# Optimization experiments

Hardware: AMD Instinct MI355X
Metric: run time of the kernel (lower is better)

Reference implementation:

```python
import jax, jax.numpy as jnp
import numpy as np


def log_g(x):
    # log of g(x) = where(x>=0, x+0.5, sigmoid(x)), computed stably in log space
    return jnp.where(x >= 0, jnp.log(jax.nn.relu(x) + 0.5), -jax.nn.softplus(-x))


def setup_inputs() -> dict:
    key = jax.random.key(0)
    k1, k2 = jax.random.split(key)
    B, S, D = 4, 4096, 1024
    x = jax.random.normal(k1, (B, S, D), dtype=jnp.float32)
    W_hg = jax.random.normal(k2, (2 * D, D), dtype=jnp.float32) * (1.0 / np.sqrt(D))
    return {"x": x, "W_hg": W_hg}


def reference(x, W_hg):
    # x: [B, S, D], W_hg: [2D, D]
    hg = jnp.einsum('bsd,ed->bse', x, W_hg)  # [B, S, 2D]
    hidden, gate = jnp.split(hg, 2, axis=-1)

    log_coeffs = -jax.nn.softplus(gate)       # log(1 - z)
    log_z = -jax.nn.softplus(-gate)            # log(z)
    log_values = log_z + log_g(hidden)

    # Heinsen associative scan in log space along seq axis
    a_star = jnp.cumsum(log_coeffs, axis=1)
    log_h0_plus_b_star = jax.lax.cumlogsumexp(log_values - a_star, axis=1)
    log_h = a_star + log_h0_plus_b_star
    out = jnp.exp(log_h)  # [B, S, D]; to_out is Identity (expansion_factor=1.0)
    return out
```

## Files before the change

### kernel.cpp

```cpp
#include <hip/hip_runtime.h>
#include <stdint.h>

#define B_ 4
#define S_ 4096
#define D_ 1024
#define E_ 2048
#define K_ 1024
#define M_ (B_*S_)
#define SEG 64
#define NSEG (S_/SEG)

typedef __bf16 bf16x8 __attribute__((ext_vector_type(8)));
typedef float  f32x4  __attribute__((ext_vector_type(4)));
typedef _Float16 f16x2 __attribute__((ext_vector_type(2)));

__device__ __forceinline__ unsigned short f2bf(float f) {
    union { float f; unsigned int u; } x; x.f = f;
    unsigned int u = x.u;
    return (unsigned short)((u + 0x7fffu + ((u >> 16) & 1u)) >> 16);
}

__device__ __forceinline__ void gload16(const void* g, void* l) {
    __builtin_amdgcn_global_load_lds(
        (const __attribute__((address_space(1))) void*)(uintptr_t)g,
        (__attribute__((address_space(3))) void*)(uintptr_t)l,
        16, 0, 0);
}

__device__ __forceinline__ unsigned int packCV(float hid, float gat) {
    float e  = __expf(gat);
    float c  = __builtin_amdgcn_rcpf(1.f + e);
    float gg = (hid >= 0.f) ? (hid + 0.5f)
                            : __builtin_amdgcn_rcpf(1.f + __expf(-hid));
    float v  = (1.f - c) * gg;
    union { f16x2 h; unsigned int u; } pk;
    pk.h[0] = (_Float16)c; pk.h[1] = (_Float16)v;
    return pk.u;
}

__global__ void cvt_xw(const float* __restrict__ x, unsigned short* __restrict__ xb,
                       const float* __restrict__ w, unsigned short* __restrict__ wb) {
    int b = blockIdx.x;
    if (b < 16384) {
        int i = (b * 256 + threadIdx.x) * 4;
        float4 f = *(const float4*)(x + i);
        ushort4 o;
        o.x = f2bf(f.x); o.y = f2bf(f.y); o.z = f2bf(f.z); o.w = f2bf(f.w);
        *(ushort4*)(xb + i) = o;
    } else {
        int i = ((b - 16384) * 256 + threadIdx.x) * 4;
        int r = i >> 10;
        int k = i & 1023;
        int d = r >> 1, g = r & 1;
        const float* src = w + (size_t)(g * D_ + d) * K_ + k;
        float4 f = *(const float4*)src;
        ushort4 o;
        o.x = f2bf(f.x); o.y = f2bf(f.y); o.z = f2bf(f.z); o.w = f2bf(f.w);
        *(ushort4*)(wb + i) = o;
    }
}

#define BM 128
#define BN 128
#define BK 32

__global__ __launch_bounds__(256, 2)
void gemm_ep(const unsigned short* __restrict__ xb,
             const unsigned short* __restrict__ wb,
             unsigned int* __restrict__ cv,
             float2* __restrict__ segCV) {
    __shared__ unsigned short As[BM * BK];
    __shared__ unsigned short Bs[BN * BK];
    __shared__ __align__(16) unsigned int Ep[4][64][36];

    const int l    = blockIdx.x;
    const int xcd  = l & 7;
    const int r    = l >> 3;
    const int sub  = r >> 6;
    const int win  = r & 63;
    const int eB   = (sub & 1) * 8 + (win & 7);
    const int mB   = xcd * 16 + (sub >> 1) * 8 + (win >> 3);
    const int mBase = mB * BM;
    const int eBase = eB * BN;

    const int tid  = threadIdx.x;
    const int lane = tid & 63;
    const int w    = tid >> 6;
    const int waveM = (w >> 1) * 64;
    const int waveN = (w & 1) * 64;

    f32x4 acc[4][4] = {};

    const int row0 = tid >> 2, cu = tid & 3;
    const unsigned short* aG0 = xb + (size_t)(mBase + row0) * K_ + cu * 8;
    const unsigned short* aG1 = aG0 + (size_t)64 * K_;
    const unsigned short* bG0 = wb + (size_t)(eBase + row0) * K_ + cu * 8;
    const unsigned short* bG1 = bG0 + (size_t)64 * K_;
    unsigned short* aL0 = As + (size_t)(w * 64) * 8;
    unsigned short* aL1 = As + (size_t)(256 + w * 64) * 8;
    unsigned short* bL0 = Bs + (size_t)(w * 64) * 8;
    unsigned short* bL1 = Bs + (size_t)(256 + w * 64) * 8;

    const int mrow = lane & 15;
    const int kg   = (lane >> 4) * 8;

    for (int k0 = 0; k0 < K_; k0 += BK) {
        __syncthreads();
        gload16(aG0 + k0, aL0);
        gload16(aG1 + k0, aL1);
        gload16(bG0 + k0, bL0);
        gload16(bG1 + k0, bL1);
        __syncthreads();

        bf16x8 af[4], bfr[4];
#pragma unroll
        for (int i = 0; i < 4; i++)
            af[i] = *(const bf16x8*)(As + (size_t)(waveM + i * 16 + mrow) * BK + kg);
#pragma unroll
        for (int j = 0; j < 4; j++)
            bfr[j] = *(const bf16x8*)(Bs + (size_t)(waveN + j * 16 + mrow) * BK + kg);
#pragma unroll
        for (int i = 0; i < 4; i++)
#pragma unroll
            for (int j = 0; j < 4; j++)
                acc[i][j] = __builtin_amdgcn_mfma_f32_16x16x32_bf16(af[i], bfr[j], acc[i][j], 0, 0, 0);
    }

    const int q    = lane >> 4;
    const int odd  = lane & 1;
    const int colL = (lane & 15) >> 1;
    unsigned int* EpW = &Ep[w][0][0];

#pragma unroll
    for (int i = 0; i < 4; i++) {
#pragma unroll
        for (int j = 0; j < 4; j++) {
            float o0 = __shfl_xor(acc[i][j][0], 1, 64);
            float o1 = __shfl_xor(acc[i][j][1], 1, 64);
            float o2 = __shfl_xor(acc[i][j][2], 1, 64);
            float o3 = __shfl_xor(acc[i][j][3], 1, 64);
            float m0 = odd ? acc[i][j][2] : acc[i][j][0];
            float m1 = odd ? acc[i][j][3] : acc[i][j][1];
            float p0 = odd ? o2 : o0;
            float p1 = odd ? o3 : o1;
            float h0 = odd ? p0 : m0, g0 = odd ? m0 : p0;
            float h1 = odd ? p1 : m1, g1 = odd ? m1 : p1;
            int row = i * 16 + q * 4 + odd * 2;
            int col = j * 8 + colL;
            EpW[(row    ) * 36 + col] = packCV(h0, g0);
            EpW[(row + 1) * 36 + col] = packCV(h1, g1);
        }
    }
    const int srow = lane >> 3;
    const int schk = lane & 7;
    const size_t dBaseS = (size_t)((eBase + waveN) >> 1) + schk * 4;
#pragma unroll
    for (int gph = 0; gph < 8; gph++) {
        int row = gph * 8 + srow;
        uint4 valq = *(const uint4*)&EpW[row * 36 + schk * 4];
        size_t m = (size_t)(mBase + waveM + row);
        *(uint4*)(cv + m * D_ + dBaseS) = valq;
    }

    __syncthreads();
    float* scratch = (float*)As;

    {
        const int dl = tid & 63;
        const int qt = tid >> 6;
        const int wq = (qt >> 1) * 2 + (dl >> 5);
        const int rBase = (qt & 1) * 32;
        const int c = dl & 31;
        const unsigned int* src = &Ep[wq][rBase][c];
        float C = 1.f, V = 0.f;
#pragma unroll 8
        for (int rr = 0; rr < 32; rr++) {
            union { unsigned int u; f16x2 h; } uu;
            uu.u = src[rr * 36];
            float cc = (float)uu.h[0], vv = (float)uu.h[1];
            V = fmaf(cc, V, vv);
            C *= cc;
        }
        scratch[(qt * 64 + dl) * 2 + 0] = C;
        scratch[(qt * 64 + dl) * 2 + 1] = V;
    }
    __syncthreads();
    if (tid < 128) {
        const int k  = tid >> 6;
        const int dl = tid & 63;
        float C0 = scratch[((2 * k    ) * 64 + dl) * 2 + 0];
        float V0 = scratch[((2 * k    ) * 64 + dl) * 2 + 1];
        float C1 = scratch[((2 * k + 1) * 64 + dl) * 2 + 0];
        float V1 = scratch[((2 * k + 1) * 64 + dl) * 2 + 1];
        int bj = mB * 2 + k;
        int dg = (eBase >> 1) + dl;
        segCV[(size_t)bj * D_ + dg] = make_float2(C0 * C1, fmaf(C1, V0, V1));
    }
}

__global__ void seg_scan(const float2* __restrict__ segCV, float* __restrict__ segH) {
    int b = blockIdx.x;
    int d = blockIdx.y * 256 + threadIdx.x;
    float h = 0.f;
    for (int j0 = 0; j0 < NSEG; j0 += 8) {
        float2 s[8];
#pragma unroll
        for (int t = 0; t < 8; t++)
            s[t] = segCV[(size_t)(b * NSEG + j0 + t) * D_ + d];
#pragma unroll
        for (int t = 0; t < 8; t++) {
            segH[(size_t)(b * NSEG + j0 + t) * D_ + d] = h;
            h = fmaf(s[t].x, h, s[t].y);
        }
    }
}

__global__ void seg_apply(const uint2* __restrict__ cv2,
                          const float2* __restrict__ segH2, float2* __restrict__ out2) {
    const int bj = blockIdx.x;
    const int p  = blockIdx.y * 256 + threadIdx.x;

    float2 hs = segH2[(size_t)bj * (D_ / 2) + p];
    float h0 = hs.x, h1 = hs.y;
    size_t base = (size_t)bj * SEG * (D_ / 2) + p;
    for (int s0 = 0; s0 < SEG; s0 += 8) {
        uint2 u[8];
#pragma unroll
        for (int t = 0; t < 8; t++)
            u[t] = cv2[base + (size_t)(s0 + t) * (D_ / 2)];
        float2 o[8];
#pragma unroll
        for (int t = 0; t < 8; t++) {
            union { unsigned int u; f16x2 h; } a, b; a.u = u[t].x; b.u = u[t].y;
            h0 = fmaf((float)a.h[0], h0, (float)a.h[1]);
            h1 = fmaf((float)b.h[0], h1, (float)b.h[1]);
            o[t] = make_float2(h0, h1);
        }
#pragma unroll
        for (int t = 0; t < 8; t++)
            out2[base + (size_t)(s0 + t) * (D_ / 2)] = o[t];
    }
}

extern "C" void kernel_launch(void* const* d_in, const int* in_sizes, int n_in,
                              void* d_out, int out_size, void* d_ws, size_t ws_size,
                              hipStream_t stream) {
    const float* x = (const float*)d_in[0];
    const float* wmat = (const float*)d_in[1];
    float* out = (float*)d_out;
    char* ws = (char*)d_ws;

    unsigned short* xb = (unsigned short*)(ws);
    unsigned short* wb = (unsigned short*)(ws + (32u << 20));
    unsigned int*   cv = (unsigned int*)(ws + (36u << 20));
    float2*      segCV = (float2*)(ws + (100u << 20));
    float*        segH = (float*)(ws + (102u << 20));

    cvt_xw<<<18432, 256, 0, stream>>>(x, xb, wmat, wb);

    gemm_ep<<<2048, 256, 0, stream>>>(xb, wb, cv, segCV);

    dim3 gs(B_, D_ / 256);
    seg_scan<<<gs, 256, 0, stream>>>((const float2*)segCV, segH);

    dim3 ga(B_ * NSEG, D_ / 512);
    seg_apply<<<ga, 256, 0, stream>>>((const uint2*)cv, (const float2*)segH,
                                      (float2*)out);
}
```

Baseline: 232.5 us.

## Fuse scan into GEMM epilogue using cross-block decoupled lookback chain

The separate segment-scan and apply kernels are removed. Each GEMM block now publishes its 128-row aggregate (C,V) to a global array with release atomics, waits on all earlier row-blocks of the same batch and channel group, and writes the final output straight from LDS. This drops the cv intermediate write/read round trip and two kernel launches. In exchange it adds serial spin-waiting between blocks that depends on dispatch order, with a risk of stalls or deadlock if earlier blocks are not resident, and the block order no longer follows the previous XCD-aware L2 swizzle.

```diff
diff --git a/kernel.cpp b/kernel.cpp
--- a/kernel.cpp
+++ b/kernel.cpp
@@ -7,8 +7,8 @@
 #define E_ 2048
 #define K_ 1024
 #define M_ (B_*S_)
-#define SEG 64
-#define NSEG (S_/SEG)
+#define NCHAIN 32
+#define SENT 0xFFFFFFFFFFFFFFFFull
 
 typedef __bf16 bf16x8 __attribute__((ext_vector_type(8)));
 typedef float  f32x4  __attribute__((ext_vector_type(4)));
@@ -39,7 +39,8 @@
 }
 
 __global__ void cvt_xw(const float* __restrict__ x, unsigned short* __restrict__ xb,
-                       const float* __restrict__ w, unsigned short* __restrict__ wb) {
+                       const float* __restrict__ w, unsigned short* __restrict__ wb,
+                       unsigned long long* __restrict__ segAgg) {
     int b = blockIdx.x;
     if (b < 16384) {
         int i = (b * 256 + threadIdx.x) * 4;
@@ -47,7 +48,7 @@
         ushort4 o;
         o.x = f2bf(f.x); o.y = f2bf(f.y); o.z = f2bf(f.z); o.w = f2bf(f.w);
         *(ushort4*)(xb + i) = o;
-    } else {
+    } else if (b < 18432) {
         int i = ((b - 16384) * 256 + threadIdx.x) * 4;
         int r = i >> 10;
         int k = i & 1023;
@@ -57,6 +58,9 @@
         ushort4 o;
         o.x = f2bf(f.x); o.y = f2bf(f.y); o.z = f2bf(f.z); o.w = f2bf(f.w);
         *(ushort4*)(wb + i) = o;
+    } else {
+        int i = (b - 18432) * 256 + threadIdx.x;
+        segAgg[i] = SENT;
     }
 }
 
@@ -65,21 +69,19 @@
 #define BK 32
 
 __global__ __launch_bounds__(256, 2)
-void gemm_ep(const unsigned short* __restrict__ xb,
-             const unsigned short* __restrict__ wb,
-             unsigned int* __restrict__ cv,
-             float2* __restrict__ segCV) {
+void gemm_fused(const unsigned short* __restrict__ xb,
+                const unsigned short* __restrict__ wb,
+                unsigned long long* __restrict__ segAgg,
+                float* __restrict__ out) {
     __shared__ unsigned short As[BM * BK];
     __shared__ unsigned short Bs[BN * BK];
     __shared__ __align__(16) unsigned int Ep[4][64][36];
 
-    const int l    = blockIdx.x;
-    const int xcd  = l & 7;
-    const int r    = l >> 3;
-    const int sub  = r >> 6;
-    const int win  = r & 63;
-    const int eB   = (sub & 1) * 8 + (win & 7);
-    const int mB   = xcd * 16 + (sub >> 1) * 8 + (win >> 3);
+    const int ord  = blockIdx.x;
+    const int eB   = ord & 15;
+    const int bat  = (ord >> 4) & 3;
+    const int sIx  = ord >> 6;
+    const int mB   = bat * NCHAIN + sIx;
     const int mBase = mB * BM;
     const int eBase = eB * BN;
 
@@ -151,94 +153,88 @@
             EpW[(row + 1) * 36 + col] = packCV(h1, g1);
         }
     }
-    const int srow = lane >> 3;
-    const int schk = lane & 7;
-    const size_t dBaseS = (size_t)((eBase + waveN) >> 1) + schk * 4;
-#pragma unroll
-    for (int gph = 0; gph < 8; gph++) {
-        int row = gph * 8 + srow;
-        uint4 valq = *(const uint4*)&EpW[row * 36 + schk * 4];
-        size_t m = (size_t)(mBase + waveM + row);
-        *(uint4*)(cv + m * D_ + dBaseS) = valq;
-    }
 
     __syncthreads();
     float* scratch = (float*)As;
-
+    float* hpre    = scratch + 512;
+
+    const int dl = tid & 63;
+    const int qt = tid >> 6;
+    const int wq = (qt >> 1) * 2 + (dl >> 5);
+    const int rB = (qt & 1) * 32;
+    const int cc_ = dl & 31;
+    const unsigned int* src = &Ep[wq][rB][cc_];
     {
-        const int dl = tid & 63;
-        const int qt = tid >> 6;
-        const int wq = (qt >> 1) * 2 + (dl >> 5);
-        const int rBase = (qt & 1) * 32;
-        const int c = dl & 31;
-        const unsigned int* src = &Ep[wq][rBase][c];
         float C = 1.f, V = 0.f;
 #pragma unroll 8
         for (int rr = 0; rr < 32; rr++) {
             union { unsigned int u; f16x2 h; } uu;
             uu.u = src[rr * 36];
-            float cc = (float)uu.h[0], vv = (float)uu.h[1];
-            V = fmaf(cc, V, vv);
-            C *= cc;
+            float cv_c = (float)uu.h[0], cv_v = (float)uu.h[1];
+            V = fmaf(cv_c, V, cv_v);
+            C *= cv_c;
         }
         scratch[(qt * 64 + dl) * 2 + 0] = C;
         scratch[(qt * 64 + dl) * 2 + 1] = V;
     }
     __syncthreads();
-    if (tid < 128) {
-        const int k  = tid >> 6;
-        const int dl = tid & 63;
-        float C0 = scratch[((2 * k    ) * 64 + dl) * 2 + 0];
-        float V0 = scratch[((2 * k    ) * 64 + dl) * 2 + 1];
-        float C1 = scratch[((2 * k + 1) * 64 + dl) * 2 + 0];
-        float V1 = scratch[((2 * k + 1) * 64 + dl) * 2 + 1];
-        int bj = mB * 2 + k;
-        int dg = (eBase >> 1) + dl;
-        segCV[(size_t)bj * D_ + dg] = make_float2(C0 * C1, fmaf(C1, V0, V1));
-    }
-}
-
-__global__ void seg_scan(const float2* __restrict__ segCV, float* __restrict__ segH) {
-    int b = blockIdx.x;
-    int d = blockIdx.y * 256 + threadIdx.x;
-    float h = 0.f;
-    for (int j0 = 0; j0 < NSEG; j0 += 8) {
-        float2 s[8];
-#pragma unroll
-        for (int t = 0; t < 8; t++)
-            s[t] = segCV[(size_t)(b * NSEG + j0 + t) * D_ + d];
-#pragma unroll
-        for (int t = 0; t < 8; t++) {
-            segH[(size_t)(b * NSEG + j0 + t) * D_ + d] = h;
-            h = fmaf(s[t].x, h, s[t].y);
-        }
-    }
-}
-
-__global__ void seg_apply(const uint2* __restrict__ cv2,
-                          const float2* __restrict__ segH2, float2* __restrict__ out2) {
-    const int bj = blockIdx.x;
-    const int p  = blockIdx.y * 256 + threadIdx.x;
-
-    float2 hs = segH2[(size_t)bj * (D_ / 2) + p];
-    float h0 = hs.x, h1 = hs.y;
-    size_t base = (size_t)bj * SEG * (D_ / 2) + p;
-    for (int s0 = 0; s0 < SEG; s0 += 8) {
-        uint2 u[8];
-#pragma unroll
-        for (int t = 0; t < 8; t++)
-            u[t] = cv2[base + (size_t)(s0 + t) * (D_ / 2)];
-        float2 o[8];
-#pragma unroll
-        for (int t = 0; t < 8; t++) {
-            union { unsigned int u; f16x2 h; } a, b; a.u = u[t].x; b.u = u[t].y;
-            h0 = fmaf((float)a.h[0], h0, (float)a.h[1]);
-            h1 = fmaf((float)b.h[0], h1, (float)b.h[1]);
-            o[t] = make_float2(h0, h1);
-        }
-#pragma unroll
-        for (int t = 0; t < 8; t++)
-            out2[base + (size_t)(s0 + t) * (D_ / 2)] = o[t];
+
+    if (tid < 64) {
+        float C0 = scratch[(0 * 64 + tid) * 2], V0 = scratch[(0 * 64 + tid) * 2 + 1];
+        float C1 = scratch[(1 * 64 + tid) * 2], V1 = scratch[(1 * 64 + tid) * 2 + 1];
+        float C2 = scratch[(2 * 64 + tid) * 2], V2 = scratch[(2 * 64 + tid) * 2 + 1];
+        float C3 = scratch[(3 * 64 + tid) * 2], V3 = scratch[(3 * 64 + tid) * 2 + 1];
+        float Cb = (C0 * C1) * (C2 * C3);
+        float Vb = fmaf(C3, fmaf(C2, fmaf(C1, V0, V1), V2), V3);
+        union { unsigned long long u; float f[2]; } pk;
+        pk.f[0] = Cb; pk.f[1] = Vb;
+        __hip_atomic_store(&segAgg[(size_t)ord * 64 + tid], pk.u,
+                           __ATOMIC_RELEASE, __HIP_MEMORY_SCOPE_AGENT);
+        __threadfence();
+
+        float h = 0.f;
+        const size_t chanB = (size_t)(ord & 63) * 64 + tid;
+#pragma unroll 1
+        for (int t0 = 0; t0 < NCHAIN; t0 += 8) {
+            if (t0 >= sIx) break;
+            unsigned long long vb[8];
+#pragma unroll
+            for (int k = 0; k < 8; k++)
+                vb[k] = (t0 + k < sIx)
+                    ? __hip_atomic_load(&segAgg[(size_t)(t0 + k) * 4096 + chanB],
+                                        __ATOMIC_RELAXED, __HIP_MEMORY_SCOPE_AGENT)
+                    : 0x3f800000ull;
+#pragma unroll
+            for (int k = 0; k < 8; k++) {
+                if (t0 + k < sIx) {
+                    while (vb[k] == SENT)
+                        vb[k] = __hip_atomic_load(&segAgg[(size_t)(t0 + k) * 4096 + chanB],
+                                                  __ATOMIC_RELAXED, __HIP_MEMORY_SCOPE_AGENT);
+                }
+            }
+#pragma unroll
+            for (int k = 0; k < 8; k++) {
+                union { unsigned long long u; float f[2]; } qd; qd.u = vb[k];
+                h = fmaf(qd.f[0], h, qd.f[1]);
+            }
+        }
+        hpre[tid] = h;
+    }
+    __syncthreads();
+
+    {
+        float h = hpre[dl];
+        if (qt > 0) h = fmaf(scratch[(0 * 64 + dl) * 2], h, scratch[(0 * 64 + dl) * 2 + 1]);
+        if (qt > 1) h = fmaf(scratch[(1 * 64 + dl) * 2], h, scratch[(1 * 64 + dl) * 2 + 1]);
+        if (qt > 2) h = fmaf(scratch[(2 * 64 + dl) * 2], h, scratch[(2 * 64 + dl) * 2 + 1]);
+        float* outp = out + (size_t)(mBase + qt * 32) * D_ + (eB * 64 + dl);
+#pragma unroll 8
+        for (int rr = 0; rr < 32; rr++) {
+            union { unsigned int u; f16x2 hh; } uu;
+            uu.u = src[rr * 36];
+            h = fmaf((float)uu.hh[0], h, (float)uu.hh[1]);
+            outp[(size_t)rr * D_] = h;
+        }
     }
 }
 
@@ -252,18 +248,8 @@
 
     unsigned short* xb = (unsigned short*)(ws);
     unsigned short* wb = (unsigned short*)(ws + (32u << 20));
-    unsigned int*   cv = (unsigned int*)(ws + (36u << 20));
-    float2*      segCV = (float2*)(ws + (100u << 20));
-    float*        segH = (float*)(ws + (102u << 20));
-
-    cvt_xw<<<18432, 256, 0, stream>>>(x, xb, wmat, wb);
-
-    gemm_ep<<<2048, 256, 0, stream>>>(xb, wb, cv, segCV);
-
-    dim3 gs(B_, D_ / 256);
-    seg_scan<<<gs, 256, 0, stream>>>((const float2*)segCV, segH);
-
-    dim3 ga(B_ * NSEG, D_ / 512);
-    seg_apply<<<ga, 256, 0, stream>>>((const uint2*)cv, (const float2*)segH,
-                                      (float2*)out);
-}
+    unsigned long long* segAgg = (unsigned long long*)(ws + (36u << 20));
+
+    cvt_xw<<<18944, 256, 0, stream>>>(x, xb, wmat, wb, segAgg);
+    gemm_fused<<<2048, 256, 0, stream>>>(xb, wb, segAgg, out);
+}
```

New measurement: 258.4 us. 1.11x slower.
